# Performance work log

Hardware: AMD Instinct MI355X
Metric: run time of the kernel (lower is better)

## Reference

```python
import jax, jax.numpy as jnp
import numpy as np

D_MODEL, D_Q, D_K, D_V, N = 1024, 128, 128, 128, 8192

def setup_inputs() -> dict:
    key = jax.random.key(0)
    ks = jax.random.split(key, 7)
    s = 1.0 / np.sqrt(D_MODEL)
    return {
        "x": jax.random.normal(ks[0], (N, D_MODEL), dtype=jnp.float32),
        "Wq": jax.random.uniform(ks[1], (D_MODEL, D_Q), jnp.float32, -s, s),
        "bq": jax.random.uniform(ks[2], (D_Q,), jnp.float32, -s, s),
        "Wk": jax.random.uniform(ks[3], (D_MODEL, D_K), jnp.float32, -s, s),
        "bk": jax.random.uniform(ks[4], (D_K,), jnp.float32, -s, s),
        "Wv": jax.random.uniform(ks[5], (D_MODEL, D_V), jnp.float32, -s, s),
        "bv": jax.random.uniform(ks[6], (D_V,), jnp.float32, -s, s),
    }

def reference(x, Wq, bq, Wk, bk, Wv, bv):
    q = x @ Wq + bq          # [N, d_q]
    k = x @ Wk + bk          # [N, d_k]
    v = x @ Wv + bv          # [N, d_v]
    scale = jnp.sqrt(jnp.asarray(q.shape[-1], q.dtype))
    scores = (q @ k.T) / scale          # [N, N]
    attn = jax.nn.softmax(scores, axis=1)  # matches nn.Softmax(dim=1) on 2D
    return attn @ v                     # [N, d_v]
```

## Files before the change

kernel.cpp:

```cpp
#include <hip/hip_runtime.h>


typedef __attribute__((ext_vector_type(8))) short bf16x8;
typedef __attribute__((ext_vector_type(4))) float f32x4;

#define NTOK 8192
#define DMODEL 1024
#define DH 128
#define NSPLIT 8
#define CPS 16

__device__ __forceinline__ unsigned short f2bf(float f) {
  unsigned int u = __builtin_bit_cast(unsigned int, f);
  u += 0x7fffu + ((u >> 16) & 1u);
  return (unsigned short)(u >> 16);
}

__device__ __forceinline__ unsigned int pack2bf(float a, float b) {
  return (unsigned int)f2bf(a) | ((unsigned int)f2bf(b) << 16);
}

__device__ __forceinline__ void gl2lds16(const void* gp, void* lp) {
  const __attribute__((address_space(1))) unsigned int* g =
      (const __attribute__((address_space(1))) unsigned int*)gp;
  __attribute__((address_space(3))) unsigned int* l =
      (__attribute__((address_space(3))) unsigned int*)lp;
  __builtin_amdgcn_global_load_lds(g, l, 16, 0, 0);
}

__global__ __launch_bounds__(256) void k_build_wt(const float* __restrict__ Wq,
                                                  const float* __restrict__ Wk,
                                                  const float* __restrict__ Wv,
                                                  unsigned short* __restrict__ wt) {
  __shared__ unsigned short tile[32 * 130];
  int k0 = blockIdx.x * 32;
  int p = blockIdx.y;
  int t = threadIdx.x;
  const float* W = (p == 0) ? Wq : ((p == 1) ? Wk : Wv);
  float vscale = (p == 2) ? 0.0625f : 1.0f;
#pragma unroll
  for (int i = 0; i < 16; i++) {
    int e = i * 256 + t;
    int n = e & 127, kk = e >> 7;
    tile[kk * 130 + n] = f2bf(W[(size_t)(k0 + kk) * DH + n] * vscale);
  }
  __syncthreads();
#pragma unroll
  for (int i = 0; i < 16; i++) {
    int e = i * 256 + t;
    int kk = e & 31, n = e >> 5;
    wt[(size_t)(p * DH + n) * DMODEL + k0 + kk] = tile[kk * 130 + n];
  }
}

__global__ __launch_bounds__(256, 2) void k_qkv(const float* __restrict__ x,
                                                const unsigned short* __restrict__ wt,
                                                const float* __restrict__ bq,
                                                const float* __restrict__ bk,
                                                const float* __restrict__ bv,
                                                unsigned short* __restrict__ qs,
                                                unsigned short* __restrict__ kkv,
                                                unsigned short* __restrict__ vt) {
  __shared__ float xt[2][64 * 64];
  __shared__ unsigned short wtt[2][128 * 64];
  int mt = blockIdx.x, p = blockIdx.y;
  int tid = threadIdx.x;
  int w = tid >> 6, lane = tid & 63, l16 = lane & 15, g = lane >> 4;

#define STAGE_QKV(buf, k0)                                                     \
  {                                                                            \
    _Pragma("unroll") for (int r = 0; r < 4; r++) {                            \
      int seg = r * 4 + w;                                                     \
      int xr = seg * 4 + (lane >> 4);                                          \
      int xlc = ((lane & 15) ^ (xr & 15)) & 15;                                \
      gl2lds16(&x[(size_t)(mt * 64 + xr) * DMODEL + (k0) + xlc * 4],           \
               &xt[buf][seg * 256]);                                           \
      int wc = seg * 8 + (lane >> 3);                                          \
      int wlc = ((lane & 7) ^ (wc & 7)) & 7;                                   \
      gl2lds16(&wt[(size_t)(p * DH + wc) * DMODEL + (k0) + wlc * 8],           \
               &wtt[buf][seg * 512]);                                          \
    }                                                                          \
  }

  f32x4 zero = {0.f, 0.f, 0.f, 0.f};
  f32x4 acc[8];
#pragma unroll
  for (int i = 0; i < 8; i++) acc[i] = zero;

  STAGE_QKV(0, 0);
  int arow = w * 16 + l16;
  for (int kt2 = 0; kt2 < 16; kt2++) {
    int b = kt2 & 1;
    __syncthreads();
    if (kt2 < 15) STAGE_QKV(b ^ 1, (kt2 + 1) * 64);

    bf16x8 a[2];
#pragma unroll
    for (int half = 0; half < 2; half++) {
      int lc0 = half * 8 + g * 2;
      const f32x4 u0 = *(const f32x4*)&xt[b][arow * 64 + ((lc0 ^ l16) & 15) * 4];
      const f32x4 u1 = *(const f32x4*)&xt[b][arow * 64 + (((lc0 + 1) ^ l16) & 15) * 4];
      union { unsigned int u[4]; bf16x8 v; } pk;
      pk.u[0] = pack2bf(u0[0], u0[1]);
      pk.u[1] = pack2bf(u0[2], u0[3]);
      pk.u[2] = pack2bf(u1[0], u1[1]);
      pk.u[3] = pack2bf(u1[2], u1[3]);
      a[half] = pk.v;
    }
#pragma unroll
    for (int nt = 0; nt < 8; nt++) {
      int col = nt * 16 + l16;
#pragma unroll
      for (int half = 0; half < 2; half++) {
        int lc = half * 4 + g;
        bf16x8 bf = *(const bf16x8*)&wtt[b][col * 64 + ((lc ^ (col & 7)) & 7) * 8];
        acc[nt] = __builtin_amdgcn_mfma_f32_16x16x32_bf16(a[half], bf, acc[nt], 0, 0, 0);
      }
    }
  }
#undef STAGE_QKV

  const float* bias = (p == 0) ? bq : ((p == 1) ? bk : bv);
  float mult = (p == 0) ? (0.08838834764831845f * 1.44269504088896340f) : 1.0f;
  if (p < 2) {
    unsigned short* outp = (p == 0) ? qs : kkv;
#pragma unroll
    for (int nt = 0; nt < 8; nt++) {
      int col = nt * 16 + l16;
      float bsv = bias[col];
#pragma unroll
      for (int r = 0; r < 4; r++) {
        int row = mt * 64 + w * 16 + g * 4 + r;
        outp[(size_t)row * DH + col] = f2bf((acc[nt][r] + bsv) * mult);
      }
    }
  } else {
#pragma unroll
    for (int nt = 0; nt < 8; nt++) {
      int col = nt * 16 + l16;
      float bsv = bias[col] * 0.0625f;
      int row0 = mt * 64 + w * 16 + g * 4;
      uint2 uv;
      uv.x = pack2bf(acc[nt][0] + bsv, acc[nt][1] + bsv);
      uv.y = pack2bf(acc[nt][2] + bsv, acc[nt][3] + bsv);
      *(uint2*)(&vt[(size_t)col * NTOK + row0]) = uv;
    }
  }
}

__global__ __launch_bounds__(256, 2) void k_flash(const unsigned short* __restrict__ qs,
                                                  const unsigned short* __restrict__ kkv,
                                                  const unsigned short* __restrict__ vt,
                                                  _Float16* __restrict__ opart,
                                                  float* __restrict__ lpart) {
  __shared__ unsigned short kt[2][64 * 128];
  __shared__ unsigned short vtl[2][128 * 64];
  __shared__ unsigned short pscr[4 * 2 * 1024];
  int sp = blockIdx.x, qt = blockIdx.y;
  int tid = threadIdx.x;
  int w = tid >> 6, lane = tid & 63, l16 = lane & 15, g = lane >> 4;
  int swz2 = (l16 & 7) ^ ((l16 >> 3) << 1);

  bf16x8 qf[2][4];
  int qbase = qt * 128 + w * 32;
#pragma unroll
  for (int q2 = 0; q2 < 2; q2++)
#pragma unroll
    for (int f = 0; f < 4; f++)
      qf[q2][f] = *(const bf16x8*)(&qs[(size_t)(qbase + q2 * 16 + l16) * DH + f * 32 + g * 8]);

  int pcK[4], pcV[2], pcP[2];
#pragma unroll
  for (int f = 0; f < 4; f++) {
    int lc = f * 4 + g;
    pcK[f] = (lc & 8) | ((lc ^ l16) & 7);
  }
#pragma unroll
  for (int kb = 0; kb < 2; kb++) {
    int lc = kb * 4 + g;
    pcV[kb] = (lc ^ l16) & 7;
    pcP[kb] = (lc ^ swz2) & 7;
  }

#define STAGE_FLASH(buf, chunk)                                                 \
  {                                                                             \
    int key0 = (chunk) * 64;                                                    \
    _Pragma("unroll") for (int ii = 0; ii < 4; ii++) {                          \
      int i = w * 4 + ii;                                                       \
      int krow = 4 * i + (lane >> 4);                                           \
      int klc = ((lane & 15) & 8) | (((lane & 15) ^ krow) & 7);                 \
      gl2lds16(&kkv[(size_t)(key0 + krow) * DH + klc * 8], &kt[buf][i * 512]);  \
      int vrow = 8 * i + (lane >> 3);                                           \
      int vlc = ((lane & 7) ^ vrow) & 7;                                        \
      gl2lds16(&vt[(size_t)vrow * NTOK + key0 + vlc * 8], &vtl[buf][i * 512]);  \
    }                                                                           \
  }

  f32x4 zero = {0.f, 0.f, 0.f, 0.f};
  f32x4 o[2][8];
#pragma unroll
  for (int q2 = 0; q2 < 2; q2++)
#pragma unroll
    for (int dt = 0; dt < 8; dt++) o[q2][dt] = zero;
  float l[2] = {0.f, 0.f};

  int c0 = sp * CPS;
  STAGE_FLASH(0, c0);

  for (int it = 0; it < CPS; it++) {
    int b = it & 1;
    __syncthreads();
    if (it + 1 < CPS) STAGE_FLASH(b ^ 1, c0 + it + 1);

    f32x4 s[2][4];
#pragma unroll
    for (int q2 = 0; q2 < 2; q2++)
#pragma unroll
      for (int mt = 0; mt < 4; mt++) s[q2][mt] = zero;
#pragma unroll
    for (int mt = 0; mt < 4; mt++) {
      bf16x8 kf[4];
#pragma unroll
      for (int f = 0; f < 4; f++)
        kf[f] = *(const bf16x8*)(&kt[b][(mt * 16 + l16) * 128 + pcK[f] * 8]);
#pragma unroll
      for (int f = 0; f < 4; f++) {
        s[0][mt] = __builtin_amdgcn_mfma_f32_16x16x32_bf16(kf[f], qf[0][f], s[0][mt], 0, 0, 0);
        s[1][mt] = __builtin_amdgcn_mfma_f32_16x16x32_bf16(kf[f], qf[1][f], s[1][mt], 0, 0, 0);
      }
    }

#pragma unroll
    for (int q2 = 0; q2 < 2; q2++) {
      unsigned short* pw = &pscr[(w * 2 + q2) * 1024];
      float ssum = 0.f;
#pragma unroll
      for (int mt = 0; mt < 4; mt++) {
        float p0 = __builtin_amdgcn_exp2f(s[q2][mt][0]);
        float p1 = __builtin_amdgcn_exp2f(s[q2][mt][1]);
        float p2 = __builtin_amdgcn_exp2f(s[q2][mt][2]);
        float p3 = __builtin_amdgcn_exp2f(s[q2][mt][3]);
        ssum += (p0 + p1) + (p2 + p3);
        uint2 uv;
        uv.x = pack2bf(p0, p1);
        uv.y = pack2bf(p2, p3);
        int ch = ((mt * 2 + (g >> 1)) ^ swz2) & 7;
        *(uint2*)(&pw[l16 * 64 + ch * 8 + (g & 1) * 4]) = uv;
      }
      l[q2] += ssum;
    }

    bf16x8 pb[2][2];
#pragma unroll
    for (int q2 = 0; q2 < 2; q2++)
#pragma unroll
      for (int kb = 0; kb < 2; kb++)
        pb[q2][kb] = *(const bf16x8*)(&pscr[(w * 2 + q2) * 1024 + l16 * 64 + pcP[kb] * 8]);

#pragma unroll
    for (int dt = 0; dt < 8; dt++)
#pragma unroll
      for (int kb = 0; kb < 2; kb++) {
        bf16x8 vf = *(const bf16x8*)(&vtl[b][(dt * 16 + l16) * 64 + pcV[kb] * 8]);
        o[0][dt] = __builtin_amdgcn_mfma_f32_16x16x32_bf16(vf, pb[0][kb], o[0][dt], 0, 0, 0);
        o[1][dt] = __builtin_amdgcn_mfma_f32_16x16x32_bf16(vf, pb[1][kb], o[1][dt], 0, 0, 0);
      }
  }
#undef STAGE_FLASH

#pragma unroll
  for (int q2 = 0; q2 < 2; q2++) {
    l[q2] += __shfl_xor(l[q2], 16);
    l[q2] += __shfl_xor(l[q2], 32);
    int qrow = qbase + q2 * 16 + l16;
    size_t obase = ((size_t)sp * NTOK + qrow) * DH;
#pragma unroll
    for (int dt = 0; dt < 8; dt++) {
      union { _Float16 h[4]; uint2 u; } pk;
      pk.h[0] = (_Float16)o[q2][dt][0];
      pk.h[1] = (_Float16)o[q2][dt][1];
      pk.h[2] = (_Float16)o[q2][dt][2];
      pk.h[3] = (_Float16)o[q2][dt][3];
      *(uint2*)(&opart[obase + dt * 16 + g * 4]) = pk.u;
    }
    if (g == 0) lpart[sp * NTOK + qrow] = l[q2];
  }
}

__global__ __launch_bounds__(256) void k_merge(const _Float16* __restrict__ opart,
                                               const float* __restrict__ lpart,
                                               float* __restrict__ out) {
  int gid = blockIdx.x * 256 + threadIdx.x;
  int row = gid >> 6, cp = gid & 63;
  float den = 0.f, n0 = 0.f, n1 = 0.f;
#pragma unroll
  for (int s = 0; s < NSPLIT; s++) {
    den += lpart[s * NTOK + row];
    union { unsigned int u; _Float16 h[2]; } v;
    v.u = *(const unsigned int*)&opart[((size_t)s * NTOK + row) * DH + cp * 2];
    n0 += (float)v.h[0];
    n1 += (float)v.h[1];
  }
  float inv = 16.0f / den;
  *(float2*)&out[(size_t)row * DH + cp * 2] = make_float2(n0 * inv, n1 * inv);
}

extern "C" void kernel_launch(void* const* d_in, const int* in_sizes, int n_in,
                              void* d_out, int out_size, void* d_ws, size_t ws_size,
                              hipStream_t stream) {
  const float* x  = (const float*)d_in[0];
  const float* Wq = (const float*)d_in[1];
  const float* bq = (const float*)d_in[2];
  const float* Wk = (const float*)d_in[3];
  const float* bk = (const float*)d_in[4];
  const float* Wv = (const float*)d_in[5];
  const float* bv = (const float*)d_in[6];
  float* out = (float*)d_out;

  char* ws = (char*)d_ws;
  _Float16*       opart = (_Float16*)(ws);
  unsigned short* wt  = (unsigned short*)(ws + 16777216);
  unsigned short* qsb = (unsigned short*)(ws + 17563648);
  unsigned short* kkb = (unsigned short*)(ws + 19660800);
  unsigned short* vtb = (unsigned short*)(ws + 21757952);
  float* lpart = (float*)(ws + 23855104);

  k_build_wt<<<dim3(32, 3), 256, 0, stream>>>(Wq, Wk, Wv, wt);
  k_qkv<<<dim3(128, 3), 256, 0, stream>>>(x, wt, bq, bk, bv, qsb, kkb, vtb);
  k_flash<<<dim3(NSPLIT, 64), 256, 0, stream>>>(qsb, kkb, vtb, opart, lpart);
  k_merge<<<2048, 256, 0, stream>>>(opart, lpart, out);
}
```

Before: 150.4 us.

## Pre-convert x to bf16, read weights and V directly, double split count

Adds a kernel that converts x to bf16 up front, so the QKV projection stages half-width x tiles and reads the transposed weights straight from global memory instead of staging them in LDS. The flash kernel stops staging V tiles in LDS and loads V fragments directly from global, which frees shared memory so occupancy can rise to 3 blocks per CU. NSPLIT goes from 8 to 16 with half the chunks per split, and the QKV grid is reordered so the three projections of a row tile run next to each other. The extra conversion pass and round trip for x, uncached direct global loads, and a larger merge workload may offset the gains.

```diff
diff --git a/kernel.cpp b/kernel.cpp
--- a/kernel.cpp
+++ b/kernel.cpp
@@ -7,8 +7,8 @@
 #define NTOK 8192
 #define DMODEL 1024
 #define DH 128
-#define NSPLIT 8
-#define CPS 16
+#define NSPLIT 16
+#define CPS 8
 
 __device__ __forceinline__ unsigned short f2bf(float f) {
   unsigned int u = __builtin_bit_cast(unsigned int, f);
@@ -26,6 +26,18 @@
   __attribute__((address_space(3))) unsigned int* l =
       (__attribute__((address_space(3))) unsigned int*)lp;
   __builtin_amdgcn_global_load_lds(g, l, 16, 0, 0);
+}
+
+__global__ __launch_bounds__(256) void k_cvt_x(const float* __restrict__ x,
+                                               unsigned short* __restrict__ xb) {
+  int gid = blockIdx.x * 256 + threadIdx.x;
+  const float4* src = (const float4*)x;
+  float4 a = src[2 * gid];
+  float4 b = src[2 * gid + 1];
+  union { unsigned short s[8]; uint4 v; } o;
+  o.s[0] = f2bf(a.x); o.s[1] = f2bf(a.y); o.s[2] = f2bf(a.z); o.s[3] = f2bf(a.w);
+  o.s[4] = f2bf(b.x); o.s[5] = f2bf(b.y); o.s[6] = f2bf(b.z); o.s[7] = f2bf(b.w);
+  ((uint4*)xb)[gid] = o.v;
 }
 
 __global__ __launch_bounds__(256) void k_build_wt(const float* __restrict__ Wq,
@@ -53,33 +65,28 @@
   }
 }
 
-__global__ __launch_bounds__(256, 2) void k_qkv(const float* __restrict__ x,
-                                                const unsigned short* __restrict__ wt,
-                                                const float* __restrict__ bq,
-                                                const float* __restrict__ bk,
-                                                const float* __restrict__ bv,
-                                                unsigned short* __restrict__ qs,
-                                                unsigned short* __restrict__ kkv,
-                                                unsigned short* __restrict__ vt) {
-  __shared__ float xt[2][64 * 64];
-  __shared__ unsigned short wtt[2][128 * 64];
-  int mt = blockIdx.x, p = blockIdx.y;
+__global__ __launch_bounds__(256) void k_qkv(const unsigned short* __restrict__ xb,
+                                             const unsigned short* __restrict__ wt,
+                                             const float* __restrict__ bq,
+                                             const float* __restrict__ bk,
+                                             const float* __restrict__ bv,
+                                             unsigned short* __restrict__ qs,
+                                             unsigned short* __restrict__ kkv,
+                                             unsigned short* __restrict__ vt) {
+  __shared__ unsigned short xt[2][64 * 64];
+  int p = blockIdx.x, mt = blockIdx.y;
   int tid = threadIdx.x;
   int w = tid >> 6, lane = tid & 63, l16 = lane & 15, g = lane >> 4;
 
-#define STAGE_QKV(buf, k0)                                                     \
-  {                                                                            \
-    _Pragma("unroll") for (int r = 0; r < 4; r++) {                            \
-      int seg = r * 4 + w;                                                     \
-      int xr = seg * 4 + (lane >> 4);                                          \
-      int xlc = ((lane & 15) ^ (xr & 15)) & 15;                                \
-      gl2lds16(&x[(size_t)(mt * 64 + xr) * DMODEL + (k0) + xlc * 4],           \
-               &xt[buf][seg * 256]);                                           \
-      int wc = seg * 8 + (lane >> 3);                                          \
-      int wlc = ((lane & 7) ^ (wc & 7)) & 7;                                   \
-      gl2lds16(&wt[(size_t)(p * DH + wc) * DMODEL + (k0) + wlc * 8],           \
-               &wtt[buf][seg * 512]);                                          \
-    }                                                                          \
+#define STAGE_X(buf, k0)                                                    \
+  {                                                                         \
+    _Pragma("unroll") for (int ii = 0; ii < 2; ii++) {                      \
+      int i = w * 2 + ii;                                                   \
+      int row = i * 8 + (lane >> 3);                                        \
+      int pc = (lane & 7) ^ (row & 7);                                      \
+      gl2lds16(&xb[(size_t)(mt * 64 + row) * DMODEL + (k0) + pc * 8],       \
+               &xt[buf][i * 512]);                                          \
+    }                                                                       \
   }
 
   f32x4 zero = {0.f, 0.f, 0.f, 0.f};
@@ -87,38 +94,27 @@
 #pragma unroll
   for (int i = 0; i < 8; i++) acc[i] = zero;
 
-  STAGE_QKV(0, 0);
-  int arow = w * 16 + l16;
+  STAGE_X(0, 0);
+  const unsigned short* wbase = wt + (size_t)p * DH * DMODEL;
+  int arow = w * 16 + l16, r7 = l16 & 7;
+
   for (int kt2 = 0; kt2 < 16; kt2++) {
     int b = kt2 & 1;
     __syncthreads();
-    if (kt2 < 15) STAGE_QKV(b ^ 1, (kt2 + 1) * 64);
-
-    bf16x8 a[2];
-#pragma unroll
-    for (int half = 0; half < 2; half++) {
-      int lc0 = half * 8 + g * 2;
-      const f32x4 u0 = *(const f32x4*)&xt[b][arow * 64 + ((lc0 ^ l16) & 15) * 4];
-      const f32x4 u1 = *(const f32x4*)&xt[b][arow * 64 + (((lc0 + 1) ^ l16) & 15) * 4];
-      union { unsigned int u[4]; bf16x8 v; } pk;
-      pk.u[0] = pack2bf(u0[0], u0[1]);
-      pk.u[1] = pack2bf(u0[2], u0[3]);
-      pk.u[2] = pack2bf(u1[0], u1[1]);
-      pk.u[3] = pack2bf(u1[2], u1[3]);
-      a[half] = pk.v;
-    }
+    if (kt2 < 15) STAGE_X(b ^ 1, (kt2 + 1) * 64);
+
+    bf16x8 a0 = *(const bf16x8*)&xt[b][arow * 64 + ((g ^ r7) & 7) * 8];
+    bf16x8 a1 = *(const bf16x8*)&xt[b][arow * 64 + (((4 + g) ^ r7) & 7) * 8];
 #pragma unroll
     for (int nt = 0; nt < 8; nt++) {
       int col = nt * 16 + l16;
-#pragma unroll
-      for (int half = 0; half < 2; half++) {
-        int lc = half * 4 + g;
-        bf16x8 bf = *(const bf16x8*)&wtt[b][col * 64 + ((lc ^ (col & 7)) & 7) * 8];
-        acc[nt] = __builtin_amdgcn_mfma_f32_16x16x32_bf16(a[half], bf, acc[nt], 0, 0, 0);
-      }
-    }
-  }
-#undef STAGE_QKV
+      bf16x8 b0 = *(const bf16x8*)&wbase[(size_t)col * DMODEL + kt2 * 64 + g * 8];
+      bf16x8 b1 = *(const bf16x8*)&wbase[(size_t)col * DMODEL + kt2 * 64 + 32 + g * 8];
+      acc[nt] = __builtin_amdgcn_mfma_f32_16x16x32_bf16(a0, b0, acc[nt], 0, 0, 0);
+      acc[nt] = __builtin_amdgcn_mfma_f32_16x16x32_bf16(a1, b1, acc[nt], 0, 0, 0);
+    }
+  }
+#undef STAGE_X
 
   const float* bias = (p == 0) ? bq : ((p == 1) ? bk : bv);
   float mult = (p == 0) ? (0.08838834764831845f * 1.44269504088896340f) : 1.0f;
@@ -148,13 +144,12 @@
   }
 }
 
-__global__ __launch_bounds__(256, 2) void k_flash(const unsigned short* __restrict__ qs,
+__global__ __launch_bounds__(256, 3) void k_flash(const unsigned short* __restrict__ qs,
                                                   const unsigned short* __restrict__ kkv,
                                                   const unsigned short* __restrict__ vt,
                                                   _Float16* __restrict__ opart,
                                                   float* __restrict__ lpart) {
   __shared__ unsigned short kt[2][64 * 128];
-  __shared__ unsigned short vtl[2][128 * 64];
   __shared__ unsigned short pscr[4 * 2 * 1024];
   int sp = blockIdx.x, qt = blockIdx.y;
   int tid = threadIdx.x;
@@ -169,30 +164,23 @@
     for (int f = 0; f < 4; f++)
       qf[q2][f] = *(const bf16x8*)(&qs[(size_t)(qbase + q2 * 16 + l16) * DH + f * 32 + g * 8]);
 
-  int pcK[4], pcV[2], pcP[2];
+  int pcK[4], pcP[2];
 #pragma unroll
   for (int f = 0; f < 4; f++) {
     int lc = f * 4 + g;
     pcK[f] = (lc & 8) | ((lc ^ l16) & 7);
   }
 #pragma unroll
-  for (int kb = 0; kb < 2; kb++) {
-    int lc = kb * 4 + g;
-    pcV[kb] = (lc ^ l16) & 7;
-    pcP[kb] = (lc ^ swz2) & 7;
-  }
-
-#define STAGE_FLASH(buf, chunk)                                                 \
+  for (int kb = 0; kb < 2; kb++) pcP[kb] = ((kb * 4 + g) ^ swz2) & 7;
+
+#define STAGE_K(buf, chunk)                                                     \
   {                                                                             \
-    int key0 = (chunk) * 64;                                                    \
+    int key0s = (chunk) * 64;                                                   \
     _Pragma("unroll") for (int ii = 0; ii < 4; ii++) {                          \
       int i = w * 4 + ii;                                                       \
       int krow = 4 * i + (lane >> 4);                                           \
       int klc = ((lane & 15) & 8) | (((lane & 15) ^ krow) & 7);                 \
-      gl2lds16(&kkv[(size_t)(key0 + krow) * DH + klc * 8], &kt[buf][i * 512]);  \
-      int vrow = 8 * i + (lane >> 3);                                           \
-      int vlc = ((lane & 7) ^ vrow) & 7;                                        \
-      gl2lds16(&vt[(size_t)vrow * NTOK + key0 + vlc * 8], &vtl[buf][i * 512]);  \
+      gl2lds16(&kkv[(size_t)(key0s + krow) * DH + klc * 8], &kt[buf][i * 512]); \
     }                                                                           \
   }
 
@@ -205,12 +193,13 @@
   float l[2] = {0.f, 0.f};
 
   int c0 = sp * CPS;
-  STAGE_FLASH(0, c0);
+  STAGE_K(0, c0);
 
   for (int it = 0; it < CPS; it++) {
     int b = it & 1;
+    int key0 = (c0 + it) * 64;
     __syncthreads();
-    if (it + 1 < CPS) STAGE_FLASH(b ^ 1, c0 + it + 1);
+    if (it + 1 < CPS) STAGE_K(b ^ 1, c0 + it + 1);
 
     f32x4 s[2][4];
 #pragma unroll
@@ -261,12 +250,12 @@
     for (int dt = 0; dt < 8; dt++)
 #pragma unroll
       for (int kb = 0; kb < 2; kb++) {
-        bf16x8 vf = *(const bf16x8*)(&vtl[b][(dt * 16 + l16) * 64 + pcV[kb] * 8]);
+        bf16x8 vf = *(const bf16x8*)(&vt[(size_t)(dt * 16 + l16) * NTOK + key0 + kb * 32 + g * 8]);
         o[0][dt] = __builtin_amdgcn_mfma_f32_16x16x32_bf16(vf, pb[0][kb], o[0][dt], 0, 0, 0);
         o[1][dt] = __builtin_amdgcn_mfma_f32_16x16x32_bf16(vf, pb[1][kb], o[1][dt], 0, 0, 0);
       }
   }
-#undef STAGE_FLASH
+#undef STAGE_K
 
 #pragma unroll
   for (int q2 = 0; q2 < 2; q2++) {
@@ -318,15 +307,17 @@
   float* out = (float*)d_out;
 
   char* ws = (char*)d_ws;
+  unsigned short* xb    = (unsigned short*)(ws);
+  unsigned short* wt    = (unsigned short*)(ws + 16777216);
   _Float16*       opart = (_Float16*)(ws);
-  unsigned short* wt  = (unsigned short*)(ws + 16777216);
-  unsigned short* qsb = (unsigned short*)(ws + 17563648);
-  unsigned short* kkb = (unsigned short*)(ws + 19660800);
-  unsigned short* vtb = (unsigned short*)(ws + 21757952);
-  float* lpart = (float*)(ws + 23855104);
-
+  unsigned short* qsb = (unsigned short*)(ws + 33554432);
+  unsigned short* kkb = (unsigned short*)(ws + 35651584);
+  unsigned short* vtb = (unsigned short*)(ws + 37748736);
+  float* lpart = (float*)(ws + 39845888);
+
+  k_cvt_x<<<4096, 256, 0, stream>>>(x, xb);
   k_build_wt<<<dim3(32, 3), 256, 0, stream>>>(Wq, Wk, Wv, wt);
-  k_qkv<<<dim3(128, 3), 256, 0, stream>>>(x, wt, bq, bk, bv, qsb, kkb, vtb);
+  k_qkv<<<dim3(3, 128), 256, 0, stream>>>(xb, wt, bq, bk, bv, qsb, kkb, vtb);
   k_flash<<<dim3(NSPLIT, 64), 256, 0, stream>>>(qsb, kkb, vtb, opart, lpart);
   k_merge<<<2048, 256, 0, stream>>>(opart, lpart, out);
 }
```

Measured after the change: 276.0 us. 83.5% more time.
